# Kernel tuning notes

Measured on AMD Instinct MI355X. Metric: run time of the kernel, lower is better.

## Reference

```python
import jax, jax.numpy as jnp
import numpy as np

N_NEG = 60
TEMP = 0.07

def _normalize(x, axis):
    n = jnp.sqrt(jnp.sum(x * x, axis=axis, keepdims=True))
    return x / jnp.maximum(n, 1e-12)

def _grid_sample(img, grid):
    # img [B,C,H,W], grid [B,h,w,2] in [-1,1]; bilinear, padding_mode='border', align_corners=False
    B, C, H, W = img.shape
    ix = jnp.clip((grid[..., 0] + 1.0) * (W * 0.5) - 0.5, 0.0, W - 1.0)
    iy = jnp.clip((grid[..., 1] + 1.0) * (H * 0.5) - 0.5, 0.0, H - 1.0)
    x0 = jnp.floor(ix); y0 = jnp.floor(iy)
    x1 = jnp.minimum(x0 + 1.0, W - 1.0); y1 = jnp.minimum(y0 + 1.0, H - 1.0)
    wx = (ix - x0)[:, None]; wy = (iy - y0)[:, None]  # [B,1,h,w]
    imgf = img.reshape(B, C, H * W)
    hh, ww = grid.shape[1], grid.shape[2]
    def gat(yy, xx):
        idx = (yy * W + xx).astype(jnp.int32).reshape(B, 1, hh * ww)
        return jnp.take_along_axis(imgf, idx, axis=2).reshape(B, C, hh, ww)
    v00 = gat(y0, x0); v01 = gat(y0, x1); v10 = gat(y1, x0); v11 = gat(y1, x1)
    return (v00 * (1 - wx) * (1 - wy) + v01 * wx * (1 - wy)
            + v10 * (1 - wx) * wy + v11 * wx * wy)

def _forward(ref_fms, tgt_fms, target_l, target_r, queue):
    b, c, h, w = ref_fms.shape
    s = target_l.shape[-1] // w  # integer downscale factor (nearest interpolate == strided slice)
    disps_l = target_l[:, :, ::s, ::s] / float(s)   # [b,1,h,w]
    disps_r = target_r[:, :, ::s, ::s] / float(s)
    xb = jnp.broadcast_to(jnp.linspace(0.0, 1.0, w), (b, h, w))
    yb = jnp.broadcast_to(jnp.linspace(0.0, 1.0, h)[:, None], (b, h, w))

    def warp(img, disp):
        g = jnp.stack([xb + disp[:, 0] / w, yb], axis=-1)
        return _grid_sample(img, 2.0 * g - 1.0)

    # occlusion / validity mask (detached in the original)
    index = jnp.broadcast_to(jnp.arange(w, dtype=ref_fms.dtype), (b, 1, h, w))
    l2r2l = warp(warp(index, disps_r), -disps_l)
    masko = jnp.abs(index - l2r2l)[:, 0] < 3.0
    mask = masko & (disps_l[:, 0] > 0.0) & (xb - disps_l[:, 0] / w >= 0.0)
    mask = jax.lax.stop_gradient(mask).astype(ref_fms.dtype)  # [b,h,w]

    query = _normalize(ref_fms, 1)
    # positive: warp right feature to left view via disparity
    gpos = jnp.stack([xb - disps_l[:, 0] / w, yb], axis=-1)
    positive = _normalize(_grid_sample(tgt_fms, 2.0 * gpos - 1.0), 1)
    l_pos = jnp.einsum('bchw,bchw->bhw', query, positive)[..., None]

    # negatives: random integer pixel shifts around positive location
    # (no n_neg-fold repeat of tgt_fms; vmap grid_sample over the n axis instead)
    k1, k2 = jax.random.split(jax.random.key(1234))
    mag = jax.random.randint(k1, (b, h, w, N_NEG), 1, 25).astype(ref_fms.dtype)
    sgn = jnp.sign(jax.random.uniform(k2, (b, h, w, N_NEG)) - 0.5).astype(ref_fms.dtype)
    x_right = (xb - disps_l[:, 0] / w) * w
    fx = jnp.mod(x_right[..., None] + mag * sgn, float(w)) / w
    fy = fx / h  # faithful to original code (y coord reuses the normalized x coord)
    grids = jnp.moveaxis(jnp.stack([fx, fy], axis=-1), 3, 0)  # [n,b,h,w,2]
    neg = jax.vmap(lambda g: _grid_sample(tgt_fms, 2.0 * g - 1.0))(grids)  # [n,b,c,h,w]
    neg = _normalize(jnp.moveaxis(neg, 0, -1), 1)  # [b,c,h,w,n]
    l_neg = jnp.einsum('bchw,bchwn->bhwn', query, neg)

    qn = _normalize(queue, 0)  # forward re-normalizes the queue each call
    l_q = jnp.einsum('bchw,ck->bhwk', query, jax.lax.stop_gradient(qn))

    logits = jnp.concatenate([l_pos, l_neg, l_q], axis=-1) * mask[..., None]
    logits = logits.reshape(b * h * w, -1) / TEMP
    # CrossEntropyLoss with all-zero labels (positive is class 0)
    return jnp.mean(-jax.nn.log_softmax(logits, axis=-1)[:, 0])

def setup_inputs():
    key = jax.random.key(0)
    k1, k2, k3, k4, k5 = jax.random.split(key, 5)
    b, c, h, w = 2, 128, 64, 128
    H, W = 4 * h, 4 * w
    return {
        'ref_fms': jax.random.normal(k1, (b, c, h, w), jnp.float32),
        'tgt_fms': jax.random.normal(k2, (b, c, h, w), jnp.float32),
        'target_l': jax.random.uniform(k3, (b, 1, H, W), jnp.float32) * 64.0,
        'target_r': jax.random.uniform(k4, (b, 1, H, W), jnp.float32) * 64.0,
        'queue': jax.random.normal(k5, (c, 6000), jnp.float32),
    }

def reference(ref_fms, tgt_fms, target_l, target_r, queue):
    return _forward(ref_fms, tgt_fms, target_l, target_r, queue)
```

## Files before the change

### kernel.cpp

```cpp
#include <hip/hip_runtime.h>
#include <stdint.h>
#include <math.h>

#define HFM 64
#define WFM 128
#define CFM 128
#define BN 2
#define HWFM (HFM*WFM)
#define NPIX (BN*HWFM)
#define KQ 6000
#define KQP 6144
#define NNEG 60
#define NE (NPIX*NNEG)
#define EHALF_U 491520u
#define MSHIFT 15.0f
#define LOG2E 1.4426950408889634f

typedef _Float16 f16_8 __attribute__((ext_vector_type(8)));
typedef _Float16 f16_2 __attribute__((ext_vector_type(2)));
typedef float f32_4 __attribute__((ext_vector_type(4)));

__host__ __device__ __forceinline__ void threefry2x32(uint32_t k0, uint32_t k1,
                                                      uint32_t x0, uint32_t x1,
                                                      uint32_t* o0, uint32_t* o1) {
  uint32_t ks2 = k0 ^ k1 ^ 0x1BD11BDAu;
  x0 += k0; x1 += k1;
#define TFR(r) { x0 += x1; x1 = (x1 << (r)) | (x1 >> (32 - (r))); x1 ^= x0; }
  TFR(13) TFR(15) TFR(26) TFR(6)
  x0 += k1;  x1 += ks2 + 1u;
  TFR(17) TFR(29) TFR(16) TFR(24)
  x0 += ks2; x1 += k0 + 2u;
  TFR(13) TFR(15) TFR(26) TFR(6)
  x0 += k0;  x1 += k1 + 3u;
  TFR(17) TFR(29) TFR(16) TFR(24)
  x0 += k1;  x1 += ks2 + 4u;
  TFR(13) TFR(15) TFR(26) TFR(6)
  x0 += ks2; x1 += k0 + 5u;
#undef TFR
  *o0 = x0; *o1 = x1;
}

__device__ __forceinline__ void gs_coord(float t, float halfdim, float maxc,
                                         int* i0, int* i1, float* w) {
  float g = 2.0f * t - 1.0f;
  float x = (g + 1.0f) * halfdim - 0.5f;
  x = fminf(fmaxf(x, 0.0f), maxc);
  float f = floorf(x);
  *i0 = (int)f;
  *w = x - f;
  *i1 = (int)fminf(f + 1.0f, maxc);
}

__global__ __launch_bounds__(256) void k_A(
    const float* __restrict__ ref, const float* __restrict__ tgt,
    const float* __restrict__ queue,
    const float* __restrict__ target_l, const float* __restrict__ target_r,
    _Float16* __restrict__ refTf, _Float16* __restrict__ tgtTf,
    _Float16* __restrict__ queueTf, float2* __restrict__ qeb,
    float* __restrict__ maskArr, float* __restrict__ xr,
    double* __restrict__ dacc, int* __restrict__ dctr, int* __restrict__ count) {
  __shared__ float tile[64][35];
  int blk = blockIdx.x;
  int tid = threadIdx.x;
  if (blk < 64) {
    int p = blk * 256 + tid;
    int b = p >> 13;
    int rem = p & (HWFM - 1);
    int i = rem >> 7, j = rem & 127;
    const float stepx = 1.0f / 127.0f, stepy = 1.0f / 63.0f;
    float xb = (j == 127) ? 1.0f : j * stepx;
    float yb = (i == 63) ? 1.0f : i * stepy;
    const float* tl = target_l + (size_t)b * 256 * 512;
    const float* tr = target_r + (size_t)b * 256 * 512;
    float dl = tl[(4 * i) * 512 + 4 * j] * 0.25f;
    int y0i, y1i; float wy;
    gs_coord(yb, 32.0f, 63.0f, &y0i, &y1i, &wy);
    float t = xb - dl * (1.0f / 128.0f);
    int x0i, x1i; float wx;
    gs_coord(t, 64.0f, 127.0f, &x0i, &x1i, &wx);
    auto innerv = [&](int y, int x) -> float {
      float xbx = (x == 127) ? 1.0f : x * stepx;
      float drv = tr[(4 * y) * 512 + 4 * x] * 0.25f;
      float ti = xbx + drv * (1.0f / 128.0f);
      float g = 2.0f * ti - 1.0f;
      float ix2 = fminf(fmaxf((g + 1.0f) * 64.0f - 0.5f, 0.0f), 127.0f);
      float x0f = floorf(ix2);
      float wxp = ix2 - x0f;
      float x1f = fminf(x0f + 1.0f, 127.0f);
      return x0f * (1.0f - wxp) + x1f * wxp;
    };
    float v00 = innerv(y0i, x0i), v01 = innerv(y0i, x1i);
    float v10 = innerv(y1i, x0i), v11 = innerv(y1i, x1i);
    float l2r2l = v00 * (1.0f - wx) * (1.0f - wy) + v01 * wx * (1.0f - wy)
                + v10 * (1.0f - wx) * wy + v11 * wx * wy;
    bool masko = fabsf((float)j - l2r2l) < 3.0f;
    bool mk = masko && (dl > 0.0f) && (t >= 0.0f);
    maskArr[p] = mk ? 1.0f : 0.0f;
    xr[p] = t * 128.0f;
  } else if (blk < 88) {
    if (blk == 64 && tid == 0) { *dacc = 0.0; *dctr = 0; *count = 0; }
    int k = (blk - 64) * 256 + tid;
    if (k < KQP) {
      if (k >= KQ) { qeb[k] = make_float2(0.0f, -1000.0f); }
      else {
        float ss = 0.0f;
        for (int c = 0; c < CFM; c++) { float v = queue[c * KQ + k]; ss += v * v; }
        float qi = 1.0f / fmaxf(sqrtf(ss), 1e-12f);
        qeb[k] = make_float2(qi * (LOG2E / 0.07f), -MSHIFT * LOG2E);
      }
    }
  } else if (blk < 472) {
    int q = blk - 88;
    int cy = q / 192, nx = q - cy * 192;
    int n0 = nx * 32, c0 = cy * 64;
    int c = tid >> 2, qq = tid & 3;
    const float* sp = queue + (size_t)(c0 + c) * KQ + n0 + qq * 4;
    if (n0 + 32 <= KQ) {
      float4 v0 = *(const float4*)sp;
      float4 v1 = *(const float4*)(sp + 16);
      tile[c][qq * 4 + 0] = v0.x; tile[c][qq * 4 + 1] = v0.y;
      tile[c][qq * 4 + 2] = v0.z; tile[c][qq * 4 + 3] = v0.w;
      tile[c][qq * 4 + 16] = v1.x; tile[c][qq * 4 + 17] = v1.y;
      tile[c][qq * 4 + 18] = v1.z; tile[c][qq * 4 + 19] = v1.w;
    } else {
#pragma unroll
      for (int k = 0; k < 4; k++) {
        int n = n0 + qq * 4 + k;
        tile[c][qq * 4 + k] = (n < KQ) ? sp[k] : 0.0f;
        tile[c][qq * 4 + 16 + k] = (n + 16 < KQ) ? sp[16 + k] : 0.0f;
      }
    }
    __syncthreads();
    int x = tid >> 3, j8 = tid & 7;
    f16_8 o;
#pragma unroll
    for (int k = 0; k < 8; k++) o[k] = (_Float16)tile[j8 * 8 + k][x];
    *(f16_8*)(queueTf + (size_t)(n0 + x) * CFM + c0 + j8 * 8) = o;
  } else {
    int fblk = blk - 472;
    int z = fblk >> 9, rem2 = fblk & 511;
    int cy = rem2 >> 8, xt = rem2 & 255;
    int x0 = xt * 32, c0 = cy * 64;
    int arr = z >> 1, b = z & 1;
    const float* src = (arr == 0 ? ref : tgt) + (size_t)b * CFM * HWFM;
    _Float16* dst = (arr == 0 ? refTf : tgtTf) + (size_t)b * HWFM * CFM;
    int c = tid >> 2, qq = tid & 3;
    const float* sp = src + (size_t)(c0 + c) * HWFM + x0 + qq * 4;
    float4 v0 = *(const float4*)sp;
    float4 v1 = *(const float4*)(sp + 16);
    tile[c][qq * 4 + 0] = v0.x; tile[c][qq * 4 + 1] = v0.y;
    tile[c][qq * 4 + 2] = v0.z; tile[c][qq * 4 + 3] = v0.w;
    tile[c][qq * 4 + 16] = v1.x; tile[c][qq * 4 + 17] = v1.y;
    tile[c][qq * 4 + 18] = v1.z; tile[c][qq * 4 + 19] = v1.w;
    __syncthreads();
    int x = tid >> 3, j8 = tid & 7;
    f16_8 o;
#pragma unroll
    for (int k = 0; k < 8; k++) o[k] = (_Float16)tile[j8 * 8 + k][x];
    *(f16_8*)(dst + (size_t)(x0 + x) * CFM + c0 + j8 * 8) = o;
  }
}

__global__ __launch_bounds__(256) void k_B(
    const _Float16* __restrict__ refTf, const _Float16* __restrict__ tgtTf,
    _Float16* __restrict__ QTf, float* __restrict__ stats,
    const float* __restrict__ maskArr, const float* __restrict__ xr,
    float* __restrict__ S, float* __restrict__ logit0,
    int* __restrict__ count, int* __restrict__ list) {
  int blk = blockIdx.x;
  int tid = threadIdx.x;
  int lane = tid & 63;
  if (blk < 64) {
    int p = blk * 256 + tid;
    bool m = maskArr[p] > 0.0f;
    unsigned long long bits = __ballot(m);
    int nact = __popcll(bits);
    int prefix = __popcll(bits & ((1ull << lane) - 1ull));
    int base = 0;
    if (lane == 0 && nact) base = atomicAdd(count, nact);
    base = __shfl(base, 0, 64);
    if (m) list[base + prefix] = p;
  } else if (blk < 128) {
    int sub = tid >> 6;
    int xg = (blk - 64) * 4 + sub;
    int b = xg >> 7, x = xg & 127;
    int xp = min(x + 1, 127);
    int c2 = lane * 2;
    int base = b * HWFM;
    f16_2 c0  = *(const f16_2*)(tgtTf + (size_t)(base + x) * CFM + c2);
    f16_2 c1  = *(const f16_2*)(tgtTf + (size_t)(base + WFM + x) * CFM + c2);
    f16_2 c0p = *(const f16_2*)(tgtTf + (size_t)(base + xp) * CFM + c2);
    f16_2 c1p = *(const f16_2*)(tgtTf + (size_t)(base + WFM + xp) * CFM + c2);
    float a0 = (float)c0[0], a1 = (float)c0[1];
    float b0 = (float)c1[0], b1 = (float)c1[1];
    float p0 = (float)c0p[0], p1 = (float)c0p[1];
    float q0 = (float)c1p[0], q1 = (float)c1p[1];
    float s[7];
    s[0] = a0 * a0 + a1 * a1;
    s[1] = a0 * b0 + a1 * b1;
    s[2] = b0 * b0 + b1 * b1;
    s[3] = a0 * p0 + a1 * p1;
    s[4] = a0 * q0 + a1 * q1;
    s[5] = b0 * p0 + b1 * p1;
    s[6] = b0 * q0 + b1 * q1;
#pragma unroll
    for (int o = 32; o; o >>= 1)
#pragma unroll
      for (int k = 0; k < 7; k++) s[k] += __shfl_xor(s[k], o, 64);
    if (lane == 0) {
      float* st = stats + (size_t)xg * 8;
#pragma unroll
      for (int k = 0; k < 7; k++) st[k] = s[k];
      st[7] = 0.0f;
    }
  } else {
    int wave = tid >> 6;
    int p = (blk - 128) * 4 + wave;
    float mk = maskArr[p];
    if (mk == 0.0f) return;
    int b = p >> 13;
    int rem = p & (HWFM - 1);
    int i = rem >> 7;
    const float stepy = 1.0f / 63.0f;
    float yb = (i == 63) ? 1.0f : i * stepy;
    float t = xr[p] * (1.0f / 128.0f);
    int y0i, y1i; float wy;
    gs_coord(yb, 32.0f, 63.0f, &y0i, &y1i, &wy);
    int x0i, x1i; float wx;
    gs_coord(t, 64.0f, 127.0f, &x0i, &x1i, &wx);

    int c2 = lane * 2;
    f16_2 q2 = *(const f16_2*)(refTf + (size_t)p * CFM + c2);
    int bo = b * HWFM;
    f16_2 a2 = *(const f16_2*)(tgtTf + (size_t)(bo + y0i * WFM + x0i) * CFM + c2);
    f16_2 b2 = *(const f16_2*)(tgtTf + (size_t)(bo + y0i * WFM + x1i) * CFM + c2);
    f16_2 cc2 = *(const f16_2*)(tgtTf + (size_t)(bo + y1i * WFM + x0i) * CFM + c2);
    f16_2 d2 = *(const f16_2*)(tgtTf + (size_t)(bo + y1i * WFM + x1i) * CFM + c2);

    float w00 = (1.0f - wx) * (1.0f - wy), w01 = wx * (1.0f - wy);
    float w10 = (1.0f - wx) * wy,          w11 = wx * wy;
    float q0 = (float)q2[0], q1 = (float)q2[1];
    float v0 = w00 * (float)a2[0] + w01 * (float)b2[0] + w10 * (float)cc2[0] + w11 * (float)d2[0];
    float v1 = w00 * (float)a2[1] + w01 * (float)b2[1] + w10 * (float)cc2[1] + w11 * (float)d2[1];

    float s0 = q0 * q0 + q1 * q1;
    float s1 = q0 * v0 + q1 * v1;
    float s2 = v0 * v0 + v1 * v1;
#pragma unroll
    for (int o = 32; o; o >>= 1) {
      s0 += __shfl_xor(s0, o, 64);
      s1 += __shfl_xor(s1, o, 64);
      s2 += __shfl_xor(s2, o, 64);
    }
    float inv = 1.0f / fmaxf(sqrtf(s0), 1e-12f);
    f16_2 qw; qw[0] = (_Float16)(q0 * inv); qw[1] = (_Float16)(q1 * inv);
    *(f16_2*)(QTf + (size_t)p * CFM + c2) = qw;
    if (lane == 0) {
      float lpos = (s1 * inv) / fmaxf(sqrtf(s2), 1e-12f);
      float lg0 = lpos / 0.07f;
      logit0[p] = lg0;
      S[p] = expf(lg0 - MSHIFT);
    }
  }
}

__global__ __launch_bounds__(256, 4) void k_gemm(
    const _Float16* __restrict__ QTf,
    const _Float16* __restrict__ queueTf,
    const _Float16* __restrict__ tgtTf,
    const float2* __restrict__ qeb,
    float* __restrict__ S, float* __restrict__ D,
    const int* __restrict__ count, const int* __restrict__ list) {
  __shared__ _Float16 Bs[2][64 * CFM];
  __shared__ float Srow[64];
  int tid = threadIdx.x;
  int cnt = *count;
  int split = blockIdx.x & 7;
  int slot0 = (blockIdx.x >> 3) * 64;
  if (slot0 >= cnt) return;
  int wave = tid >> 6, lane = tid & 63;
  int quad = lane >> 4, l16 = lane & 15;
  int wm = wave >> 1, wn = wave & 1;
  int dbatch = split >> 2;
  int dxoff = (split & 3) * 64;

  if (tid < 64) Srow[tid] = 0.0f;

  int lrow = lane >> 4, lchunk = lane & 15;
  auto stage = [&](const _Float16* bsrc, int buf) {
#pragma unroll
    for (int i = 0; i < 4; i++) {
      int rb = wave * 16 + i * 4;
      int r = rb + lrow;
      const _Float16* g = bsrc + (size_t)r * CFM + ((lchunk ^ (r & 7)) << 3);
      __builtin_amdgcn_global_load_lds(
          (const __attribute__((address_space(1))) void*)g,
          (__attribute__((address_space(3))) void*)(&Bs[buf][rb * CFM]),
          16, 0, 0);
    }
  };
  auto bpanel = [&](int ic) -> const _Float16* {
    if (ic < 12) return queueTf + (size_t)(split * 768 + ic * 64) * CFM;
    return tgtTf + ((size_t)dbatch * HWFM + dxoff) * CFM;
  };

  stage(bpanel(0), 0);

  f16_8 Af[2][4];
  int r0 = slot0 + wm * 32;
#pragma unroll
  for (int mt = 0; mt < 2; mt++) {
    int prow = list[min(r0 + mt * 16 + l16, cnt - 1)];
    const _Float16* arow = QTf + (size_t)prow * CFM + quad * 8;
#pragma unroll
    for (int ks = 0; ks < 4; ks++)
      Af[mt][ks] = *(const f16_8*)(arow + ks * 32);
  }
  int pbv[2][4];
#pragma unroll
  for (int mt = 0; mt < 2; mt++)
#pragma unroll
    for (int r = 0; r < 4; r++)
      pbv[mt][r] = list[min(r0 + mt * 16 + quad * 4 + r, cnt - 1)] >> 13;

  __syncthreads();
  int cur = 0;
  float rowsum[2][4] = {{0.0f,0.0f,0.0f,0.0f},{0.0f,0.0f,0.0f,0.0f}};

  for (int ic = 0; ic < 13; ic++) {
    if (ic + 1 < 13) stage(bpanel(ic + 1), cur ^ 1);
    float2 qb[2];
    if (ic < 12) {
      int n0 = split * 768 + ic * 64 + wn * 32;
#pragma unroll
      for (int nt = 0; nt < 2; nt++) qb[nt] = qeb[n0 + nt * 16 + l16];
    }
    f32_4 acc[2][2];
#pragma unroll
    for (int mt = 0; mt < 2; mt++)
#pragma unroll
      for (int nt = 0; nt < 2; nt++)
        acc[mt][nt] = (f32_4){0.0f, 0.0f, 0.0f, 0.0f};
#pragma unroll
    for (int ks = 0; ks < 4; ks++) {
      f16_8 Bk[2];
#pragma unroll
      for (int nt = 0; nt < 2; nt++) {
        int brow = wn * 32 + nt * 16 + l16;
        Bk[nt] = *(const f16_8*)(&Bs[cur][brow * CFM + ((ks * 32 + quad * 8) ^ ((brow & 7) * 8))]);
      }
#pragma unroll
      for (int mt = 0; mt < 2; mt++)
#pragma unroll
        for (int nt = 0; nt < 2; nt++)
          acc[mt][nt] = __builtin_amdgcn_mfma_f32_16x16x32_f16(Af[mt][ks], Bk[nt], acc[mt][nt], 0, 0, 0);
    }
    if (ic < 12) {
#pragma unroll
      for (int nt = 0; nt < 2; nt++)
#pragma unroll
        for (int mt = 0; mt < 2; mt++)
#pragma unroll
          for (int r = 0; r < 4; r++)
            rowsum[mt][r] += exp2f(fmaf(acc[mt][nt][r], qb[nt].x, qb[nt].y));
    } else {
#pragma unroll
      for (int mt = 0; mt < 2; mt++)
#pragma unroll
        for (int nt = 0; nt < 2; nt++)
#pragma unroll
          for (int r = 0; r < 4; r++) {
            int sl = slot0 + wm * 32 + mt * 16 + quad * 4 + r;
            int colL = dxoff + wn * 32 + nt * 16 + l16;
            if (sl < cnt && pbv[mt][r] == dbatch)
              D[(size_t)sl * 256 + colL] = acc[mt][nt][r];
          }
    }
    __syncthreads();
    cur ^= 1;
  }

#pragma unroll
  for (int mt = 0; mt < 2; mt++)
#pragma unroll
    for (int r = 0; r < 4; r++) {
      float vv = rowsum[mt][r];
      vv += __shfl_xor(vv, 1);
      vv += __shfl_xor(vv, 2);
      vv += __shfl_xor(vv, 4);
      vv += __shfl_xor(vv, 8);
      rowsum[mt][r] = vv;
    }
  if (l16 == 0) {
#pragma unroll
    for (int mt = 0; mt < 2; mt++)
#pragma unroll
      for (int r = 0; r < 4; r++)
        atomicAdd(&Srow[wm * 32 + mt * 16 + quad * 4 + r], rowsum[mt][r]);
  }
  __syncthreads();
  if (tid < 64) {
    int pr = slot0 + tid;
    if (pr < cnt) atomicAdd(&S[list[pr]], Srow[tid]);
  }
}

__global__ __launch_bounds__(256) void k_negatives_lite(
    const float* __restrict__ D, const float* __restrict__ stats,
    const float* __restrict__ xr, float* __restrict__ S,
    const int* __restrict__ count, const int* __restrict__ list,
    uint32_t k1a, uint32_t k1b, uint32_t k2a, uint32_t k2b) {
  int tid = threadIdx.x;
  int wave = tid >> 6, lane = tid & 63;
  int cnt = *count;
  int slot = blockIdx.x * 4 + wave;
  if (slot >= cnt) return;
  int p = list[slot];
  int b = p >> 13;
  float esum = 0.0f;
  if (lane < NNEG) {
    uint32_t e = (uint32_t)(p * NNEG + lane);
    uint32_t h0, h1;
    threefry2x32(k1a, k1b, e, e + (uint32_t)NE, &h0, &h1);
    uint32_t off = ((h0 % 24u) * 16u + (h1 % 24u)) % 24u;
    float mag = (float)(1u + off);
    uint32_t ub;
    {
      uint32_t a, bm;
      if (e < EHALF_U) { threefry2x32(k2a, k2b, e, e + EHALF_U, &a, &bm); ub = a; }
      else             { threefry2x32(k2a, k2b, e - EHALF_U, e, &a, &bm); ub = bm; }
    }
    float u = __uint_as_float((ub >> 9) | 0x3F800000u) - 1.0f;
    float sg = (u > 0.5f) ? 1.0f : ((u < 0.5f) ? -1.0f : 0.0f);

    float v = xr[p] + mag * sg;
    float r = fmodf(v, 128.0f);
    if (r < 0.0f) r += 128.0f;
    float fx = r * (1.0f / 128.0f);
    float fy = fx * (1.0f / 64.0f);
    int x0i, x1i, y0i, y1i; float wx, wy;
    gs_coord(fx, 64.0f, 127.0f, &x0i, &x1i, &wx);
    gs_coord(fy, 32.0f, 63.0f, &y0i, &y1i, &wy);

    const float* Dp = D + (size_t)slot * 256;
    float d00 = Dp[x0i], d01 = Dp[x1i];
    float d10 = Dp[128 + x0i], d11 = Dp[128 + x1i];
    float u0 = 1.0f - wy, u1 = wy;
    float dv0 = u0 * d00 + u1 * d10;
    float dv1 = u0 * d01 + u1 * d11;
    float dot = (1.0f - wx) * dv0 + wx * dv1;

    const float* st0 = stats + (size_t)(b * 128 + x0i) * 8;
    const float* st1 = stats + (size_t)(b * 128 + x1i) * 8;
    float4 sa = *(const float4*)st0;
    float4 sb = *(const float4*)(st0 + 4);
    float4 sc = *(const float4*)st1;
    float a0 = u0 * u0, a1 = u0 * u1, a2 = u1 * u1;
    float nB0 = a0 * sa.x + 2.0f * a1 * sa.y + a2 * sa.z;
    float nB1 = a0 * sc.x + 2.0f * a1 * sc.y + a2 * sc.z;
    float cB  = a0 * sa.w + a1 * (sb.x + sb.y) + a2 * sb.z;
    float wx0 = 1.0f - wx;
    float nsq = wx0 * wx0 * nB0 + 2.0f * wx * wx0 * cB + wx * wx * nB1;
    float ln = dot / fmaxf(sqrtf(fmaxf(nsq, 0.0f)), 1e-12f);
    esum = __expf(ln * (1.0f / 0.07f) - MSHIFT);
  }
#pragma unroll
  for (int o = 32; o; o >>= 1) esum += __shfl_xor(esum, o, 64);
  if (lane == 0) atomicAdd(&S[p], esum);
}

__global__ __launch_bounds__(1024) void k_finalize(
    const float* __restrict__ S, const float* __restrict__ logit0,
    const float* __restrict__ maskArr, float* __restrict__ out,
    double* __restrict__ dacc, int* __restrict__ dctr) {
  int tid = threadIdx.x;
  const float cmask = logf(6061.0f);
  int p = blockIdx.x * 1024 + tid;
  float term = (maskArr[p] > 0.0f) ? (logf(S[p]) + MSHIFT - logit0[p]) : cmask;
  double acc = (double)term;
#pragma unroll
  for (int off = 32; off; off >>= 1) acc += __shfl_down(acc, off, 64);
  __shared__ double sd[16];
  if ((tid & 63) == 0) sd[tid >> 6] = acc;
  __syncthreads();
  if (tid == 0) {
    double tot = 0.0;
    for (int w = 0; w < 16; w++) tot += sd[w];
    atomicAdd(dacc, tot);
    __threadfence();
    int old = atomicAdd(dctr, 1);
    if (old == 15) {
      __threadfence();
      out[0] = (float)(*(volatile double*)dacc / (double)NPIX);
    }
  }
}

extern "C" void kernel_launch(void* const* d_in, const int* in_sizes, int n_in,
                              void* d_out, int out_size, void* d_ws, size_t ws_size,
                              hipStream_t stream) {
  const float* ref   = (const float*)d_in[0];
  const float* tgt   = (const float*)d_in[1];
  const float* tl    = (const float*)d_in[2];
  const float* tr    = (const float*)d_in[3];
  const float* queue = (const float*)d_in[4];
  float* out = (float*)d_out;
  float* ws = (float*)d_ws;

  float2* qeb = (float2*)ws;
  float* S    = ws + 12288;
  float* lg0  = ws + 28672;
  float* mk   = ws + 45056;
  float* xr   = ws + 61440;
  int* count  = (int*)(ws + 77824);
  double* dacc = (double*)(ws + 77826);
  int* dctr   = (int*)(ws + 77828);
  int* list   = (int*)(ws + 77840);
  _Float16* QTf     = (_Float16*)(ws + 94464);
  _Float16* queueTf = (_Float16*)(ws + 1143040);
  _Float16* tgtTf   = (_Float16*)(ws + 1536256);
  _Float16* refTf   = (_Float16*)(ws + 2584832);
  float* stats = ws + 3633408;
  float* D     = ws + 3635456;

  uint32_t b0o0, b0o1, b1o0, b1o1;
  threefry2x32(0u, 1234u, 0u, 2u, &b0o0, &b0o1);
  threefry2x32(0u, 1234u, 1u, 3u, &b1o0, &b1o1);
  uint32_t k1a = b0o0, k1b = b1o0, k2a = b0o1, k2b = b1o1;

  k_A<<<dim3(2520), dim3(256), 0, stream>>>(ref, tgt, queue, tl, tr,
                                            refTf, tgtTf, queueTf, qeb, mk, xr,
                                            dacc, dctr, count);
  k_B<<<dim3(128 + 4096), dim3(256), 0, stream>>>(refTf, tgtTf, QTf, stats,
                                                  mk, xr, S, lg0, count, list);
  k_gemm<<<dim3(2048), dim3(256), 0, stream>>>(QTf, queueTf, tgtTf, qeb,
                                               S, D, count, list);
  k_negatives_lite<<<dim3(NPIX / 4), dim3(256), 0, stream>>>(D, stats, xr, S, count, list,
                                                             k1a, k1b, k2a, k2b);
  k_finalize<<<dim3(16), dim3(1024), 0, stream>>>(S, lg0, mk, out, dacc, dctr);
}
```

Baseline: 117.1 us.

## Use single barrier per GEMM panel and fuse finalize into negatives kernel

```diff
diff --git a/kernel.cpp b/kernel.cpp
--- a/kernel.cpp
+++ b/kernel.cpp
@@ -324,17 +324,24 @@
       pbv[mt][r] = list[min(r0 + mt * 16 + quad * 4 + r, cnt - 1)] >> 13;
 
   __syncthreads();
-  int cur = 0;
   float rowsum[2][4] = {{0.0f,0.0f,0.0f,0.0f},{0.0f,0.0f,0.0f,0.0f}};
 
+#pragma unroll
   for (int ic = 0; ic < 13; ic++) {
-    if (ic + 1 < 13) stage(bpanel(ic + 1), cur ^ 1);
+    const int cur = ic & 1;
     float2 qb[2];
     if (ic < 12) {
       int n0 = split * 768 + ic * 64 + wn * 32;
-#pragma unroll
-      for (int nt = 0; nt < 2; nt++) qb[nt] = qeb[n0 + nt * 16 + l16];
-    }
+      qb[0] = qeb[n0 + l16];
+      qb[1] = qeb[n0 + 16 + l16];
+    }
+    if (ic > 0) {
+      if (ic < 12) asm volatile("s_waitcnt vmcnt(2)" ::: "memory");
+      else         asm volatile("s_waitcnt vmcnt(0)" ::: "memory");
+      asm volatile("s_waitcnt lgkmcnt(0)" ::: "memory");
+      __builtin_amdgcn_s_barrier();
+    }
+    if (ic + 1 < 13) stage(bpanel(ic + 1), cur ^ 1);
     f32_4 acc[2][2];
 #pragma unroll
     for (int mt = 0; mt < 2; mt++)
@@ -376,8 +383,6 @@
               D[(size_t)sl * 256 + colL] = acc[mt][nt][r];
           }
     }
-    __syncthreads();
-    cur ^= 1;
   }
 
 #pragma unroll
@@ -405,95 +410,97 @@
   }
 }
 
-__global__ __launch_bounds__(256) void k_negatives_lite(
+__global__ __launch_bounds__(256) void k_negatives_fin(
     const float* __restrict__ D, const float* __restrict__ stats,
     const float* __restrict__ xr, float* __restrict__ S,
     const int* __restrict__ count, const int* __restrict__ list,
+    const float* __restrict__ logit0, const float* __restrict__ maskArr,
+    float* __restrict__ out, int* __restrict__ dctr,
     uint32_t k1a, uint32_t k1b, uint32_t k2a, uint32_t k2b) {
   int tid = threadIdx.x;
   int wave = tid >> 6, lane = tid & 63;
   int cnt = *count;
   int slot = blockIdx.x * 4 + wave;
-  if (slot >= cnt) return;
-  int p = list[slot];
-  int b = p >> 13;
-  float esum = 0.0f;
-  if (lane < NNEG) {
-    uint32_t e = (uint32_t)(p * NNEG + lane);
-    uint32_t h0, h1;
-    threefry2x32(k1a, k1b, e, e + (uint32_t)NE, &h0, &h1);
-    uint32_t off = ((h0 % 24u) * 16u + (h1 % 24u)) % 24u;
-    float mag = (float)(1u + off);
-    uint32_t ub;
-    {
-      uint32_t a, bm;
-      if (e < EHALF_U) { threefry2x32(k2a, k2b, e, e + EHALF_U, &a, &bm); ub = a; }
-      else             { threefry2x32(k2a, k2b, e - EHALF_U, e, &a, &bm); ub = bm; }
-    }
-    float u = __uint_as_float((ub >> 9) | 0x3F800000u) - 1.0f;
-    float sg = (u > 0.5f) ? 1.0f : ((u < 0.5f) ? -1.0f : 0.0f);
-
-    float v = xr[p] + mag * sg;
-    float r = fmodf(v, 128.0f);
-    if (r < 0.0f) r += 128.0f;
-    float fx = r * (1.0f / 128.0f);
-    float fy = fx * (1.0f / 64.0f);
-    int x0i, x1i, y0i, y1i; float wx, wy;
-    gs_coord(fx, 64.0f, 127.0f, &x0i, &x1i, &wx);
-    gs_coord(fy, 32.0f, 63.0f, &y0i, &y1i, &wy);
-
-    const float* Dp = D + (size_t)slot * 256;
-    float d00 = Dp[x0i], d01 = Dp[x1i];
-    float d10 = Dp[128 + x0i], d11 = Dp[128 + x1i];
-    float u0 = 1.0f - wy, u1 = wy;
-    float dv0 = u0 * d00 + u1 * d10;
-    float dv1 = u0 * d01 + u1 * d11;
-    float dot = (1.0f - wx) * dv0 + wx * dv1;
-
-    const float* st0 = stats + (size_t)(b * 128 + x0i) * 8;
-    const float* st1 = stats + (size_t)(b * 128 + x1i) * 8;
-    float4 sa = *(const float4*)st0;
-    float4 sb = *(const float4*)(st0 + 4);
-    float4 sc = *(const float4*)st1;
-    float a0 = u0 * u0, a1 = u0 * u1, a2 = u1 * u1;
-    float nB0 = a0 * sa.x + 2.0f * a1 * sa.y + a2 * sa.z;
-    float nB1 = a0 * sc.x + 2.0f * a1 * sc.y + a2 * sc.z;
-    float cB  = a0 * sa.w + a1 * (sb.x + sb.y) + a2 * sb.z;
-    float wx0 = 1.0f - wx;
-    float nsq = wx0 * wx0 * nB0 + 2.0f * wx * wx0 * cB + wx * wx * nB1;
-    float ln = dot / fmaxf(sqrtf(fmaxf(nsq, 0.0f)), 1e-12f);
-    esum = __expf(ln * (1.0f / 0.07f) - MSHIFT);
-  }
-#pragma unroll
-  for (int o = 32; o; o >>= 1) esum += __shfl_xor(esum, o, 64);
-  if (lane == 0) atomicAdd(&S[p], esum);
-}
-
-__global__ __launch_bounds__(1024) void k_finalize(
-    const float* __restrict__ S, const float* __restrict__ logit0,
-    const float* __restrict__ maskArr, float* __restrict__ out,
-    double* __restrict__ dacc, int* __restrict__ dctr) {
-  int tid = threadIdx.x;
-  const float cmask = logf(6061.0f);
-  int p = blockIdx.x * 1024 + tid;
-  float term = (maskArr[p] > 0.0f) ? (logf(S[p]) + MSHIFT - logit0[p]) : cmask;
-  double acc = (double)term;
-#pragma unroll
-  for (int off = 32; off; off >>= 1) acc += __shfl_down(acc, off, 64);
-  __shared__ double sd[16];
-  if ((tid & 63) == 0) sd[tid >> 6] = acc;
+  if (slot < cnt) {
+    int p = list[slot];
+    int b = p >> 13;
+    float esum = 0.0f;
+    if (lane < NNEG) {
+      uint32_t e = (uint32_t)(p * NNEG + lane);
+      uint32_t h0, h1;
+      threefry2x32(k1a, k1b, e, e + (uint32_t)NE, &h0, &h1);
+      uint32_t off = ((h0 % 24u) * 16u + (h1 % 24u)) % 24u;
+      float mag = (float)(1u + off);
+      uint32_t ub;
+      {
+        uint32_t a, bm;
+        if (e < EHALF_U) { threefry2x32(k2a, k2b, e, e + EHALF_U, &a, &bm); ub = a; }
+        else             { threefry2x32(k2a, k2b, e - EHALF_U, e, &a, &bm); ub = bm; }
+      }
+      float u = __uint_as_float((ub >> 9) | 0x3F800000u) - 1.0f;
+      float sg = (u > 0.5f) ? 1.0f : ((u < 0.5f) ? -1.0f : 0.0f);
+
+      float v = xr[p] + mag * sg;
+      float r = fmodf(v, 128.0f);
+      if (r < 0.0f) r += 128.0f;
+      float fx = r * (1.0f / 128.0f);
+      float fy = fx * (1.0f / 64.0f);
+      int x0i, x1i, y0i, y1i; float wx, wy;
+      gs_coord(fx, 64.0f, 127.0f, &x0i, &x1i, &wx);
+      gs_coord(fy, 32.0f, 63.0f, &y0i, &y1i, &wy);
+
+      const float* Dp = D + (size_t)slot * 256;
+      float d00 = Dp[x0i], d01 = Dp[x1i];
+      float d10 = Dp[128 + x0i], d11 = Dp[128 + x1i];
+      float u0 = 1.0f - wy, u1 = wy;
+      float dv0 = u0 * d00 + u1 * d10;
+      float dv1 = u0 * d01 + u1 * d11;
+      float dot = (1.0f - wx) * dv0 + wx * dv1;
+
+      const float* st0 = stats + (size_t)(b * 128 + x0i) * 8;
+      const float* st1 = stats + (size_t)(b * 128 + x1i) * 8;
+      float4 sa = *(const float4*)st0;
+      float4 sb = *(const float4*)(st0 + 4);
+      float4 sc = *(const float4*)st1;
+      float a0 = u0 * u0, a1 = u0 * u1, a2 = u1 * u1;
+      float nB0 = a0 * sa.x + 2.0f * a1 * sa.y + a2 * sa.z;
+      float nB1 = a0 * sc.x + 2.0f * a1 * sc.y + a2 * sc.z;
+      float cB  = a0 * sa.w + a1 * (sb.x + sb.y) + a2 * sb.z;
+      float wx0 = 1.0f - wx;
+      float nsq = wx0 * wx0 * nB0 + 2.0f * wx * wx0 * cB + wx * wx * nB1;
+      float ln = dot / fmaxf(sqrtf(fmaxf(nsq, 0.0f)), 1e-12f);
+      esum = __expf(ln * (1.0f / 0.07f) - MSHIFT);
+    }
+#pragma unroll
+    for (int o = 32; o; o >>= 1) esum += __shfl_xor(esum, o, 64);
+    if (lane == 0) atomicAdd(&S[p], esum);
+  }
+
+  __shared__ bool is_last;
+  __shared__ double sd[4];
   __syncthreads();
   if (tid == 0) {
-    double tot = 0.0;
-    for (int w = 0; w < 16; w++) tot += sd[w];
-    atomicAdd(dacc, tot);
     __threadfence();
     int old = atomicAdd(dctr, 1);
-    if (old == 15) {
-      __threadfence();
-      out[0] = (float)(*(volatile double*)dacc / (double)NPIX);
-    }
-  }
+    is_last = (old == (int)gridDim.x - 1);
+  }
+  __syncthreads();
+  if (!is_last) return;
+  __threadfence();
+
+  const float cmask = logf(6061.0f);
+  double acc = 0.0;
+  for (int k = 0; k < NPIX / 256; k++) {
+    int p = k * 256 + tid;
+    float term = (maskArr[p] > 0.0f) ? (logf(S[p]) + MSHIFT - logit0[p]) : cmask;
+    acc += (double)term;
+  }
+#pragma unroll
+  for (int off = 32; off; off >>= 1) acc += __shfl_down(acc, off, 64);
+  if (lane == 0) sd[wave] = acc;
+  __syncthreads();
+  if (tid == 0)
+    out[0] = (float)((sd[0] + sd[1] + sd[2] + sd[3]) / (double)NPIX);
 }
 
 extern "C" void kernel_launch(void* const* d_in, const int* in_sizes, int n_in,
@@ -535,7 +542,7 @@
                                                   mk, xr, S, lg0, count, list);
   k_gemm<<<dim3(2048), dim3(256), 0, stream>>>(QTf, queueTf, tgtTf, qeb,
                                                S, D, count, list);
-  k_negatives_lite<<<dim3(NPIX / 4), dim3(256), 0, stream>>>(D, stats, xr, S, count, list,
-                                                             k1a, k1b, k2a, k2b);
-  k_finalize<<<dim3(16), dim3(1024), 0, stream>>>(S, lg0, mk, out, dacc, dctr);
-}
+  k_negatives_fin<<<dim3(NPIX / 4), dim3(256), 0, stream>>>(D, stats, xr, S, count, list,
+                                                            lg0, mk, out, dctr,
+                                                            k1a, k1b, k2a, k2b);
+}
```

Result: slower. 271.5 us (+131.9%).

## Shrink GEMM block tile to 32 rows with 32-column B subpanels

Applied to the files above, without the earlier changes.

```diff
diff --git a/kernel.cpp b/kernel.cpp
--- a/kernel.cpp
+++ b/kernel.cpp
@@ -271,26 +271,26 @@
     const float2* __restrict__ qeb,
     float* __restrict__ S, float* __restrict__ D,
     const int* __restrict__ count, const int* __restrict__ list) {
-  __shared__ _Float16 Bs[2][64 * CFM];
-  __shared__ float Srow[64];
+  __shared__ _Float16 Bs[2][32 * CFM];
+  __shared__ float Srow[32];
   int tid = threadIdx.x;
   int cnt = *count;
   int split = blockIdx.x & 7;
-  int slot0 = (blockIdx.x >> 3) * 64;
+  int slot0 = (blockIdx.x >> 3) * 32;
   if (slot0 >= cnt) return;
   int wave = tid >> 6, lane = tid & 63;
   int quad = lane >> 4, l16 = lane & 15;
-  int wm = wave >> 1, wn = wave & 1;
+  int wn = wave;
   int dbatch = split >> 2;
   int dxoff = (split & 3) * 64;
 
-  if (tid < 64) Srow[tid] = 0.0f;
+  if (tid < 32) Srow[tid] = 0.0f;
 
   int lrow = lane >> 4, lchunk = lane & 15;
   auto stage = [&](const _Float16* bsrc, int buf) {
 #pragma unroll
-    for (int i = 0; i < 4; i++) {
-      int rb = wave * 16 + i * 4;
+    for (int i = 0; i < 2; i++) {
+      int rb = wave * 8 + i * 4;
       int r = rb + lrow;
       const _Float16* g = bsrc + (size_t)r * CFM + ((lchunk ^ (r & 7)) << 3);
       __builtin_amdgcn_global_load_lds(
@@ -303,14 +303,17 @@
     if (ic < 12) return queueTf + (size_t)(split * 768 + ic * 64) * CFM;
     return tgtTf + ((size_t)dbatch * HWFM + dxoff) * CFM;
   };
-
-  stage(bpanel(0), 0);
+  auto bsub = [&](int sc) -> const _Float16* {
+    int ic = sc >> 1, half = sc & 1;
+    return bpanel(ic) + (size_t)(half * 32) * CFM;
+  };
+
+  stage(bsub(0), 0);
 
   f16_8 Af[2][4];
-  int r0 = slot0 + wm * 32;
 #pragma unroll
   for (int mt = 0; mt < 2; mt++) {
-    int prow = list[min(r0 + mt * 16 + l16, cnt - 1)];
+    int prow = list[min(slot0 + mt * 16 + l16, cnt - 1)];
     const _Float16* arow = QTf + (size_t)prow * CFM + quad * 8;
 #pragma unroll
     for (int ks = 0; ks < 4; ks++)
@@ -321,85 +324,61 @@
   for (int mt = 0; mt < 2; mt++)
 #pragma unroll
     for (int r = 0; r < 4; r++)
-      pbv[mt][r] = list[min(r0 + mt * 16 + quad * 4 + r, cnt - 1)] >> 13;
+      pbv[mt][r] = list[min(slot0 + mt * 16 + quad * 4 + r, cnt - 1)] >> 13;
 
   __syncthreads();
   int cur = 0;
   float rowsum[2][4] = {{0.0f,0.0f,0.0f,0.0f},{0.0f,0.0f,0.0f,0.0f}};
 
-  for (int ic = 0; ic < 13; ic++) {
-    if (ic + 1 < 13) stage(bpanel(ic + 1), cur ^ 1);
-    float2 qb[2];
-    if (ic < 12) {
-      int n0 = split * 768 + ic * 64 + wn * 32;
-#pragma unroll
-      for (int nt = 0; nt < 2; nt++) qb[nt] = qeb[n0 + nt * 16 + l16];
-    }
-    f32_4 acc[2][2];
-#pragma unroll
-    for (int mt = 0; mt < 2; mt++)
-#pragma unroll
-      for (int nt = 0; nt < 2; nt++)
-        acc[mt][nt] = (f32_4){0.0f, 0.0f, 0.0f, 0.0f};
+  for (int sc = 0; sc < 26; sc++) {
+    int ic = sc >> 1, half = sc & 1;
+    float2 qb;
+    bool isD = (ic == 12);
+    if (!isD) {
+      int n0 = split * 768 + ic * 64 + half * 32 + (wn & 1) * 16;
+      qb = qeb[n0 + l16];
+    }
+    if (sc + 1 < 26) stage(bsub(sc + 1), cur ^ 1);
+    int colgrp = wn & 1, rowgrp = wn >> 1;
+    f32_4 acc;
+    acc = (f32_4){0.0f, 0.0f, 0.0f, 0.0f};
+    f32_4 acc2 = (f32_4){0.0f, 0.0f, 0.0f, 0.0f};
 #pragma unroll
     for (int ks = 0; ks < 4; ks++) {
-      f16_8 Bk[2];
-#pragma unroll
-      for (int nt = 0; nt < 2; nt++) {
-        int brow = wn * 32 + nt * 16 + l16;
-        Bk[nt] = *(const f16_8*)(&Bs[cur][brow * CFM + ((ks * 32 + quad * 8) ^ ((brow & 7) * 8))]);
+      int brow = colgrp * 16 + l16;
+      f16_8 Bk = *(const f16_8*)(&Bs[cur][brow * CFM + ((ks * 32 + quad * 8) ^ ((brow & 7) * 8))]);
+      acc = __builtin_amdgcn_mfma_f32_16x16x32_f16(Af[rowgrp][ks], Bk, acc, 0, 0, 0);
+    }
+    (void)acc2;
+    if (!isD) {
+#pragma unroll
+      for (int r = 0; r < 4; r++)
+        rowsum[rowgrp][r] += exp2f(fmaf(acc[r], qb.x, qb.y));
+    } else {
+#pragma unroll
+      for (int r = 0; r < 4; r++) {
+        int sl = slot0 + rowgrp * 16 + quad * 4 + r;
+        int colL = dxoff + half * 32 + colgrp * 16 + l16;
+        if (sl < cnt && pbv[rowgrp][r] == dbatch)
+          D[(size_t)sl * 256 + colL] = acc[r];
       }
-#pragma unroll
-      for (int mt = 0; mt < 2; mt++)
-#pragma unroll
-        for (int nt = 0; nt < 2; nt++)
-          acc[mt][nt] = __builtin_amdgcn_mfma_f32_16x16x32_f16(Af[mt][ks], Bk[nt], acc[mt][nt], 0, 0, 0);
-    }
-    if (ic < 12) {
-#pragma unroll
-      for (int nt = 0; nt < 2; nt++)
-#pragma unroll
-        for (int mt = 0; mt < 2; mt++)
-#pragma unroll
-          for (int r = 0; r < 4; r++)
-            rowsum[mt][r] += exp2f(fmaf(acc[mt][nt][r], qb[nt].x, qb[nt].y));
-    } else {
-#pragma unroll
-      for (int mt = 0; mt < 2; mt++)
-#pragma unroll
-        for (int nt = 0; nt < 2; nt++)
-#pragma unroll
-          for (int r = 0; r < 4; r++) {
-            int sl = slot0 + wm * 32 + mt * 16 + quad * 4 + r;
-            int colL = dxoff + wn * 32 + nt * 16 + l16;
-            if (sl < cnt && pbv[mt][r] == dbatch)
-              D[(size_t)sl * 256 + colL] = acc[mt][nt][r];
-          }
     }
     __syncthreads();
     cur ^= 1;
   }
 
 #pragma unroll
-  for (int mt = 0; mt < 2; mt++)
-#pragma unroll
-    for (int r = 0; r < 4; r++) {
-      float vv = rowsum[mt][r];
-      vv += __shfl_xor(vv, 1);
-      vv += __shfl_xor(vv, 2);
-      vv += __shfl_xor(vv, 4);
-      vv += __shfl_xor(vv, 8);
-      rowsum[mt][r] = vv;
-    }
-  if (l16 == 0) {
-#pragma unroll
-    for (int mt = 0; mt < 2; mt++)
-#pragma unroll
-      for (int r = 0; r < 4; r++)
-        atomicAdd(&Srow[wm * 32 + mt * 16 + quad * 4 + r], rowsum[mt][r]);
+  for (int r = 0; r < 4; r++) {
+    int rowgrp = wn >> 1;
+    float vv = rowsum[rowgrp][r];
+    vv += __shfl_xor(vv, 1);
+    vv += __shfl_xor(vv, 2);
+    vv += __shfl_xor(vv, 4);
+    vv += __shfl_xor(vv, 8);
+    if (l16 == 0) atomicAdd(&Srow[rowgrp * 16 + quad * 4 + r], vv);
   }
   __syncthreads();
-  if (tid < 64) {
+  if (tid < 32) {
     int pr = slot0 + tid;
     if (pr < cnt) atomicAdd(&S[list[pr]], Srow[tid]);
   }
@@ -533,7 +512,7 @@
                                             dacc, dctr, count);
   k_B<<<dim3(128 + 4096), dim3(256), 0, stream>>>(refTf, tgtTf, QTf, stats,
                                                   mk, xr, S, lg0, count, list);
-  k_gemm<<<dim3(2048), dim3(256), 0, stream>>>(QTf, queueTf, tgtTf, qeb,
+  k_gemm<<<dim3(4096), dim3(256), 0, stream>>>(QTf, queueTf, tgtTf, qeb,
                                                S, D, count, list);
   k_negatives_lite<<<dim3(NPIX / 4), dim3(256), 0, stream>>>(D, stats, xr, S, count, list,
                                                              k1a, k1b, k2a, k2b);
```

Measured after the change: 180.5 us. +54.2%, slower.
